# Kernel optimization log

Hardware: AMD Instinct MI355X
Metric: run time of the kernel (lower is better)

The kernel has to match this reference:

```python
import jax, jax.numpy as jnp
import numpy as np


def setup_inputs() -> dict:
    key = jax.random.key(0)
    kq, kk, kv = jax.random.split(key, 3)
    B, L, Q, H, E = 8, 128, 8, 8, 64
    S, P = 128, 8
    queries = jax.random.normal(kq, (B, L, Q, H, E), dtype=jnp.float32)
    keys = jax.random.normal(kk, (B, S, P, H, E), dtype=jnp.float32)
    values = jax.random.normal(kv, (B, S, P, H, E), dtype=jnp.float32)
    attn_mask = jnp.zeros((1,), dtype=bool)  # unused by the module
    return {"queries": queries, "keys": keys, "values": values, "attn_mask": attn_mask}


def reference(queries, keys, values, attn_mask):
    # queries: [B,L,Q,H,E]; keys/values: [B,S,P,H,E]
    B, L, Q, H, E = queries.shape
    S, P = values.shape[1], values.shape[2]
    scale = 1.0 / np.sqrt(E).astype(np.float32)
    # scores: [B,S,P,L,Q,H]
    scores = jnp.einsum('blqhe,bsphe->bsplqh', queries, keys)
    # softmax over joint (S,P) axis
    scaled = (scale * scores).reshape(B, S * P, L, Q, H)
    attn = jax.nn.softmax(scaled, axis=1).reshape(B, S, P, L, Q, H)
    # dropout is identity in eval / with p=0.0
    V = jnp.einsum('bsphe,bsplqh->blqhe', values, attn)
    return V
```

## Files before the change

kernel.cpp:

```cpp
#include <hip/hip_runtime.h>
#include <hip/hip_bf16.h>

typedef __attribute__((ext_vector_type(4))) float f32x4;
typedef __attribute__((ext_vector_type(16))) float f32x16;
typedef __attribute__((ext_vector_type(8))) short bf16x8;
typedef __attribute__((ext_vector_type(4))) unsigned u32x4;

#define MFMA32(a, b, c) __builtin_amdgcn_mfma_f32_32x32x16_bf16(a, b, c, 0, 0, 0)
#define EXP2(x) __builtin_amdgcn_exp2f(x)

constexpr int NQ = 1024;
constexpr int NK = 1024;
constexpr int RS = 512;
constexpr int Ec = 64;
constexpr int KT = 128;
constexpr int NT = NK / KT;
constexpr float QSCALE2 = 0.125f * 1.4426950408889634f;

__device__ __forceinline__ short f2bf(float x) {
    return (short)__builtin_bit_cast(unsigned short, __float2bfloat16(x));
}

__device__ __forceinline__ bf16x8 pack2(float4 a, float4 b) {
    bf16x8 r;
    r[0] = f2bf(a.x); r[1] = f2bf(a.y); r[2] = f2bf(a.z); r[3] = f2bf(a.w);
    r[4] = f2bf(b.x); r[5] = f2bf(b.y); r[6] = f2bf(b.z); r[7] = f2bf(b.w);
    return r;
}

__device__ __forceinline__ bf16x8 pack2s(float4 a, float4 b, float s) {
    bf16x8 r;
    r[0] = f2bf(a.x * s); r[1] = f2bf(a.y * s); r[2] = f2bf(a.z * s); r[3] = f2bf(a.w * s);
    r[4] = f2bf(b.x * s); r[5] = f2bf(b.y * s); r[6] = f2bf(b.z * s); r[7] = f2bf(b.w * s);
    return r;
}

__device__ __forceinline__ unsigned cvtpk(float a, float b) {
    unsigned lo = (unsigned short)__builtin_bit_cast(unsigned short, __float2bfloat16(a));
    unsigned hi = (unsigned short)__builtin_bit_cast(unsigned short, __float2bfloat16(b));
    return lo | (hi << 16);
}

__device__ __forceinline__ void gload16(const short* src, short* dst) {
    __builtin_amdgcn_global_load_lds((const __attribute__((address_space(1))) void*)src,
                                     (__attribute__((address_space(3))) void*)dst, 16, 0, 0);
}

__global__ __launch_bounds__(256, 4)
void cvt_kv(const float* __restrict__ Kg, const float* __restrict__ Vg,
            short* __restrict__ Kbf, short* __restrict__ Vt) {
    __shared__ __attribute__((aligned(16))) short Vl[64][72];
    const int tid  = threadIdx.x;
    const int head = blockIdx.x >> 4;
    const int kb   = blockIdx.x & 15;
    const int b    = head >> 3, h = head & 7;
    const int row  = tid >> 2, q = tid & 3;

    const size_t gin = (((size_t)(b * NK + kb * 64 + row)) * 8 + h) * 64 + q * 16;
    const float4* kp = (const float4*)(Kg + gin);
    float4 k0 = kp[0], k1 = kp[1], k2 = kp[2], k3 = kp[3];
    short* kout = Kbf + ((size_t)head * NK + kb * 64 + row) * 64 + q * 16;
    ((bf16x8*)kout)[0] = pack2(k0, k1);
    ((bf16x8*)kout)[1] = pack2(k2, k3);

    const float4* vp = (const float4*)(Vg + gin);
    float4 v0 = vp[0], v1 = vp[1], v2 = vp[2], v3 = vp[3];
    const float vv[16] = {v0.x, v0.y, v0.z, v0.w, v1.x, v1.y, v1.z, v1.w,
                          v2.x, v2.y, v2.z, v2.w, v3.x, v3.y, v3.z, v3.w};
#pragma unroll
    for (int j = 0; j < 16; ++j) Vl[q * 16 + j][row] = f2bf(vv[j]);
    __syncthreads();
    short* vout = Vt + ((size_t)head * Ec + row) * NK + kb * 64 + q * 16;
    ((bf16x8*)vout)[0] = *(const bf16x8*)&Vl[row][q * 16];
    ((bf16x8*)vout)[1] = *(const bf16x8*)&Vl[row][q * 16 + 8];
}

__global__ __launch_bounds__(512, 2)
void fully_attn_kernel(const float* __restrict__ Qg, const short* __restrict__ Kbf,
                       const short* __restrict__ Vt, float* __restrict__ Og) {
    __shared__ __attribute__((aligned(16))) short Kl[2][KT][64];
    __shared__ __attribute__((aligned(16))) short Vl[2][64][KT];
    __shared__ float scrL[512];

    const int tid  = threadIdx.x;
    const int lane = tid & 63;
    const int wv   = tid >> 6;
    const int grp  = wv & 3;
    const int par  = wv >> 2;
    const int ql   = lane & 31;
    const int hi   = lane >> 5;
    const int swz  = (lane & 7) << 4;

    const int bid  = blockIdx.x;
    const int head = (bid & 7) * 8 + (bid >> 5);
    const int qb   = (bid >> 3) & 3;
    const int b    = head >> 3, h = head & 7;

    const size_t headQ = (size_t)b * NQ * RS + (size_t)h * Ec;
    const short* Kh = Kbf + (size_t)head * NK * Ec;
    const short* Vh = Vt + (size_t)head * Ec * NK;

    const int qrowA = qb * 256 + grp * 64 + ql;
    const int qrowB = qrowA + 32;
    bf16x8 qfA[4], qfB[4];
    {
        const float* qpA = Qg + headQ + (size_t)qrowA * RS;
        const float* qpB = Qg + headQ + (size_t)qrowB * RS;
#pragma unroll
        for (int j = 0; j < 4; ++j) {
            const float4* a4 = (const float4*)(qpA + j * 16 + hi * 8);
            const float4* b4 = (const float4*)(qpB + j * 16 + hi * 8);
            qfA[j] = pack2s(a4[0], a4[1], QSCALE2);
            qfB[j] = pack2s(b4[0], b4[1], QSCALE2);
        }
    }

    const int krow8 = lane >> 3;
    const int kj    = (lane & 7) ^ krow8;
    const int vrow4 = lane >> 4;

#define STAGE_K(buf, tt)                                                          \
    {                                                                             \
        _Pragma("unroll")                                                         \
        for (int s = 0; s < 2; ++s)                                               \
            gload16(Kh + (size_t)((tt) * KT + wv * 16 + s * 8 + krow8) * 64 +     \
                        kj * 8,                                                   \
                    &Kl[buf][wv * 16 + s * 8][0]);                                \
    }

#define STAGE_V(buf, tt)                                                          \
    {                                                                             \
        _Pragma("unroll")                                                         \
        for (int s = 0; s < 2; ++s)                                               \
            gload16(Vh + (size_t)(wv * 8 + s * 4 + vrow4) * NK + (tt) * KT +      \
                        (((lane & 15) ^ ((s * 4 + vrow4) & 7)) * 8),              \
                    &Vl[buf][wv * 8 + s * 4][0]);                                 \
    }

    STAGE_K(0, 0);
    STAGE_V(0, 0);
    __syncthreads();

    float lA = 0.0f, lB = 0.0f;
    f32x16 oA0 = (f32x16)(0.0f), oA1 = (f32x16)(0.0f);
    f32x16 oB0 = (f32x16)(0.0f), oB1 = (f32x16)(0.0f);

    int cur = 0;
    for (int t = 0; t < NT; ++t) {
        if (t + 1 < NT) { STAGE_K(cur ^ 1, t + 1); STAGE_V(cur ^ 1, t + 1); }

        bf16x8 kf[2][4];
#pragma unroll
        for (int kt = 0; kt < 2; ++kt) {
            const char* kr = (const char*)&Kl[cur][par * 64 + kt * 32 + ql][0];
#pragma unroll
            for (int j = 0; j < 4; ++j)
                kf[kt][j] = *(const bf16x8*)(kr + ((j * 32 + hi * 16) ^ swz));
        }
        f32x16 pA[2], pB[2];
        __builtin_amdgcn_s_setprio(1);
#pragma unroll
        for (int kt = 0; kt < 2; ++kt) {
            f32x16 a = (f32x16)(0.0f), bq = (f32x16)(0.0f);
#pragma unroll
            for (int j = 0; j < 4; ++j) {
                a  = MFMA32(kf[kt][j], qfA[j], a);
                bq = MFMA32(kf[kt][j], qfB[j], bq);
            }
            pA[kt] = a;
            pB[kt] = bq;
        }
        __builtin_amdgcn_s_setprio(0);

        bf16x8 vf0[4], vf1[4];
#pragma unroll
        for (int m = 0; m < 4; ++m) {
            const int cb = (par * 128 + m * 32 + hi * 16) ^ swz;
            vf0[m] = *(const bf16x8*)((const char*)&Vl[cur][ql][0] + cb);
            vf1[m] = *(const bf16x8*)((const char*)&Vl[cur][32 + ql][0] + cb);
        }

        {
            float rs0 = 0.f, rs1 = 0.f, rs2 = 0.f, rs3 = 0.f;
#pragma unroll
            for (int kt = 0; kt < 2; ++kt)
#pragma unroll
                for (int i = 0; i < 16; i += 4) {
                    float e0 = EXP2(pA[kt][i + 0]);
                    float e1 = EXP2(pA[kt][i + 1]);
                    float e2 = EXP2(pA[kt][i + 2]);
                    float e3 = EXP2(pA[kt][i + 3]);
                    pA[kt][i + 0] = e0; pA[kt][i + 1] = e1;
                    pA[kt][i + 2] = e2; pA[kt][i + 3] = e3;
                    rs0 += e0; rs1 += e1; rs2 += e2; rs3 += e3;
                }
            lA += (rs0 + rs1) + (rs2 + rs3);
            __builtin_amdgcn_s_setprio(1);
#pragma unroll
            for (int m = 0; m < 4; ++m) {
                const int kt = m >> 1, r0 = (m & 1) * 8;
                unsigned a0 = cvtpk(pA[kt][r0 + 0], pA[kt][r0 + 1]);
                unsigned a1 = cvtpk(pA[kt][r0 + 2], pA[kt][r0 + 3]);
                unsigned b0 = cvtpk(pA[kt][r0 + 4], pA[kt][r0 + 5]);
                unsigned b1 = cvtpk(pA[kt][r0 + 6], pA[kt][r0 + 7]);
                asm("v_permlane32_swap_b32 %0, %1" : "+v"(a0), "+v"(b0));
                asm("v_permlane32_swap_b32 %0, %1" : "+v"(a1), "+v"(b1));
                u32x4 w = {a0, a1, b0, b1};
                bf16x8 pf = __builtin_bit_cast(bf16x8, w);
                oA0 = MFMA32(vf0[m], pf, oA0);
                oA1 = MFMA32(vf1[m], pf, oA1);
            }
            __builtin_amdgcn_s_setprio(0);
        }

        {
            float rs0 = 0.f, rs1 = 0.f, rs2 = 0.f, rs3 = 0.f;
#pragma unroll
            for (int kt = 0; kt < 2; ++kt)
#pragma unroll
                for (int i = 0; i < 16; i += 4) {
                    float e0 = EXP2(pB[kt][i + 0]);
                    float e1 = EXP2(pB[kt][i + 1]);
                    float e2 = EXP2(pB[kt][i + 2]);
                    float e3 = EXP2(pB[kt][i + 3]);
                    pB[kt][i + 0] = e0; pB[kt][i + 1] = e1;
                    pB[kt][i + 2] = e2; pB[kt][i + 3] = e3;
                    rs0 += e0; rs1 += e1; rs2 += e2; rs3 += e3;
                }
            lB += (rs0 + rs1) + (rs2 + rs3);
            __builtin_amdgcn_s_setprio(1);
#pragma unroll
            for (int m = 0; m < 4; ++m) {
                const int kt = m >> 1, r0 = (m & 1) * 8;
                unsigned a0 = cvtpk(pB[kt][r0 + 0], pB[kt][r0 + 1]);
                unsigned a1 = cvtpk(pB[kt][r0 + 2], pB[kt][r0 + 3]);
                unsigned b0 = cvtpk(pB[kt][r0 + 4], pB[kt][r0 + 5]);
                unsigned b1 = cvtpk(pB[kt][r0 + 6], pB[kt][r0 + 7]);
                asm("v_permlane32_swap_b32 %0, %1" : "+v"(a0), "+v"(b0));
                asm("v_permlane32_swap_b32 %0, %1" : "+v"(a1), "+v"(b1));
                u32x4 w = {a0, a1, b0, b1};
                bf16x8 pf = __builtin_bit_cast(bf16x8, w);
                oB0 = MFMA32(vf0[m], pf, oB0);
                oB1 = MFMA32(vf1[m], pf, oB1);
            }
            __builtin_amdgcn_s_setprio(0);
        }

        __syncthreads();
        cur ^= 1;
    }

    lA += __shfl_xor(lA, 32);
    lB += __shfl_xor(lB, 32);

    float* scr = (float*)&Kl[0][0][0];
    const int qslotA = grp * 64 + ql;
    const int qslotB = qslotA + 32;
    if (par == 1) {
#pragma unroll
        for (int i = 0; i < 16; ++i) {
            scr[(hi * 16 + i) * 256 + qslotA]      = oA0[i];
            scr[(32 + hi * 16 + i) * 256 + qslotA] = oA1[i];
            scr[(hi * 16 + i) * 256 + qslotB]      = oB0[i];
            scr[(32 + hi * 16 + i) * 256 + qslotB] = oB1[i];
        }
        if (hi == 0) { scrL[qslotA] = lA; scrL[qslotB] = lB; }
    }
    __syncthreads();
    if (par == 0) {
        const float invA = 1.0f / (lA + scrL[qslotA]);
        const float invB = 1.0f / (lB + scrL[qslotB]);
        float* opA = Og + headQ + (size_t)qrowA * RS;
        float* opB = Og + headQ + (size_t)qrowB * RS;
#pragma unroll
        for (int bnk = 0; bnk < 4; ++bnk) {
            float4 sA0, sA1, sB0, sB1;
#pragma unroll
            for (int j = 0; j < 4; ++j) {
                const int i = bnk * 4 + j;
                ((float*)&sA0)[j] = (oA0[i] + scr[(hi * 16 + i) * 256 + qslotA]) * invA;
                ((float*)&sA1)[j] = (oA1[i] + scr[(32 + hi * 16 + i) * 256 + qslotA]) * invA;
                ((float*)&sB0)[j] = (oB0[i] + scr[(hi * 16 + i) * 256 + qslotB]) * invB;
                ((float*)&sB1)[j] = (oB1[i] + scr[(32 + hi * 16 + i) * 256 + qslotB]) * invB;
            }
            *(float4*)(opA + bnk * 8 + hi * 4)      = sA0;
            *(float4*)(opA + 32 + bnk * 8 + hi * 4) = sA1;
            *(float4*)(opB + bnk * 8 + hi * 4)      = sB0;
            *(float4*)(opB + 32 + bnk * 8 + hi * 4) = sB1;
        }
    }
}

extern "C" void kernel_launch(void* const* d_in, const int* in_sizes, int n_in,
                              void* d_out, int out_size, void* d_ws, size_t ws_size,
                              hipStream_t stream) {
    const float* Qg = (const float*)d_in[0];
    const float* Kg = (const float*)d_in[1];
    const float* Vg = (const float*)d_in[2];
    float* Og = (float*)d_out;

    short* Kbf = (short*)d_ws;
    short* Vt  = (short*)d_ws + (size_t)64 * NK * Ec;

    hipLaunchKernelGGL(cvt_kv, dim3(64 * 16), dim3(256), 0, stream, Kg, Vg, Kbf, Vt);
    hipLaunchKernelGGL(fully_attn_kernel, dim3(256), dim3(512), 0, stream,
                       Qg, Kbf, Vt, Og);
}
```

Before: 45.31 us.

## Halve attention block to 256 threads and double grid to 512 blocks

Each block now handles 128 query rows with 4 waves instead of 256 rows with 8 waves, and the grid doubles to 512 blocks. The K/V staging loops are widened so 4 waves fill the same shared-memory tiles, and the epilogue scratch indexing is resized. The aim is better CU coverage: 256 blocks is about one per CU on this chip, and 512 smaller blocks may balance better. The cost is that each K/V tile is loaded from global memory twice as many times overall, and each wave issues more staging loads.

```diff
diff --git a/kernel.cpp b/kernel.cpp
--- a/kernel.cpp
+++ b/kernel.cpp
@@ -75,32 +75,32 @@
     ((bf16x8*)vout)[1] = *(const bf16x8*)&Vl[row][q * 16 + 8];
 }
 
-__global__ __launch_bounds__(512, 2)
+__global__ __launch_bounds__(256, 2)
 void fully_attn_kernel(const float* __restrict__ Qg, const short* __restrict__ Kbf,
                        const short* __restrict__ Vt, float* __restrict__ Og) {
     __shared__ __attribute__((aligned(16))) short Kl[2][KT][64];
     __shared__ __attribute__((aligned(16))) short Vl[2][64][KT];
-    __shared__ float scrL[512];
+    __shared__ float scrL[128];
 
     const int tid  = threadIdx.x;
     const int lane = tid & 63;
     const int wv   = tid >> 6;
-    const int grp  = wv & 3;
-    const int par  = wv >> 2;
+    const int grp  = wv & 1;
+    const int par  = wv >> 1;
     const int ql   = lane & 31;
     const int hi   = lane >> 5;
     const int swz  = (lane & 7) << 4;
 
     const int bid  = blockIdx.x;
-    const int head = (bid & 7) * 8 + (bid >> 5);
-    const int qb   = (bid >> 3) & 3;
+    const int head = (bid & 7) * 8 + (bid >> 6);
+    const int qb   = (bid >> 3) & 7;
     const int b    = head >> 3, h = head & 7;
 
     const size_t headQ = (size_t)b * NQ * RS + (size_t)h * Ec;
     const short* Kh = Kbf + (size_t)head * NK * Ec;
     const short* Vh = Vt + (size_t)head * Ec * NK;
 
-    const int qrowA = qb * 256 + grp * 64 + ql;
+    const int qrowA = qb * 128 + grp * 64 + ql;
     const int qrowB = qrowA + 32;
     bf16x8 qfA[4], qfB[4];
     {
@@ -115,26 +115,26 @@
         }
     }
 
-    const int krow8 = lane >> 3;
-    const int kj    = (lane & 7) ^ krow8;
-    const int vrow4 = lane >> 4;
+    const int klocal = lane >> 3;
+    const int kj     = (lane & 7) ^ (klocal & 7);
+    const int vlocal = lane >> 4;
 
 #define STAGE_K(buf, tt)                                                          \
     {                                                                             \
         _Pragma("unroll")                                                         \
-        for (int s = 0; s < 2; ++s)                                               \
-            gload16(Kh + (size_t)((tt) * KT + wv * 16 + s * 8 + krow8) * 64 +     \
+        for (int s = 0; s < 4; ++s)                                               \
+            gload16(Kh + (size_t)((tt) * KT + wv * 32 + s * 8 + klocal) * 64 +    \
                         kj * 8,                                                   \
-                    &Kl[buf][wv * 16 + s * 8][0]);                                \
+                    &Kl[buf][wv * 32 + s * 8][0]);                                \
     }
 
 #define STAGE_V(buf, tt)                                                          \
     {                                                                             \
         _Pragma("unroll")                                                         \
-        for (int s = 0; s < 2; ++s)                                               \
-            gload16(Vh + (size_t)(wv * 8 + s * 4 + vrow4) * NK + (tt) * KT +      \
-                        (((lane & 15) ^ ((s * 4 + vrow4) & 7)) * 8),              \
-                    &Vl[buf][wv * 8 + s * 4][0]);                                 \
+        for (int s = 0; s < 4; ++s)                                               \
+            gload16(Vh + (size_t)(wv * 16 + s * 4 + vlocal) * NK + (tt) * KT +    \
+                        (((lane & 15) ^ ((s * 4 + vlocal) & 7)) * 8),             \
+                    &Vl[buf][wv * 16 + s * 4][0]);                                \
     }
 
     STAGE_K(0, 0);
@@ -254,22 +254,22 @@
     lB += __shfl_xor(lB, 32);
 
     float* scr = (float*)&Kl[0][0][0];
-    const int qslotA = grp * 64 + ql;
-    const int qslotB = qslotA + 32;
+    const int slotA = grp * 64 + ql;
+    const int slotB = slotA + 32;
     if (par == 1) {
 #pragma unroll
         for (int i = 0; i < 16; ++i) {
-            scr[(hi * 16 + i) * 256 + qslotA]      = oA0[i];
-            scr[(32 + hi * 16 + i) * 256 + qslotA] = oA1[i];
-            scr[(hi * 16 + i) * 256 + qslotB]      = oB0[i];
-            scr[(32 + hi * 16 + i) * 256 + qslotB] = oB1[i];
-        }
-        if (hi == 0) { scrL[qslotA] = lA; scrL[qslotB] = lB; }
+            scr[(hi * 16 + i) * 128 + slotA]      = oA0[i];
+            scr[(32 + hi * 16 + i) * 128 + slotA] = oA1[i];
+            scr[(hi * 16 + i) * 128 + slotB]      = oB0[i];
+            scr[(32 + hi * 16 + i) * 128 + slotB] = oB1[i];
+        }
+        if (hi == 0) { scrL[slotA] = lA; scrL[slotB] = lB; }
     }
     __syncthreads();
     if (par == 0) {
-        const float invA = 1.0f / (lA + scrL[qslotA]);
-        const float invB = 1.0f / (lB + scrL[qslotB]);
+        const float invA = 1.0f / (lA + scrL[slotA]);
+        const float invB = 1.0f / (lB + scrL[slotB]);
         float* opA = Og + headQ + (size_t)qrowA * RS;
         float* opB = Og + headQ + (size_t)qrowB * RS;
 #pragma unroll
@@ -278,10 +278,10 @@
 #pragma unroll
             for (int j = 0; j < 4; ++j) {
                 const int i = bnk * 4 + j;
-                ((float*)&sA0)[j] = (oA0[i] + scr[(hi * 16 + i) * 256 + qslotA]) * invA;
-                ((float*)&sA1)[j] = (oA1[i] + scr[(32 + hi * 16 + i) * 256 + qslotA]) * invA;
-                ((float*)&sB0)[j] = (oB0[i] + scr[(hi * 16 + i) * 256 + qslotB]) * invB;
-                ((float*)&sB1)[j] = (oB1[i] + scr[(32 + hi * 16 + i) * 256 + qslotB]) * invB;
+                ((float*)&sA0)[j] = (oA0[i] + scr[(hi * 16 + i) * 128 + slotA]) * invA;
+                ((float*)&sA1)[j] = (oA1[i] + scr[(32 + hi * 16 + i) * 128 + slotA]) * invA;
+                ((float*)&sB0)[j] = (oB0[i] + scr[(hi * 16 + i) * 128 + slotB]) * invB;
+                ((float*)&sB1)[j] = (oB1[i] + scr[(32 + hi * 16 + i) * 128 + slotB]) * invB;
             }
             *(float4*)(opA + bnk * 8 + hi * 4)      = sA0;
             *(float4*)(opA + 32 + bnk * 8 + hi * 4) = sA1;
@@ -303,6 +303,6 @@
     short* Vt  = (short*)d_ws + (size_t)64 * NK * Ec;
 
     hipLaunchKernelGGL(cvt_kv, dim3(64 * 16), dim3(256), 0, stream, Kg, Vg, Kbf, Vt);
-    hipLaunchKernelGGL(fully_attn_kernel, dim3(256), dim3(512), 0, stream,
+    hipLaunchKernelGGL(fully_attn_kernel, dim3(512), dim3(256), 0, stream,
                        Qg, Kbf, Vt, Og);
 }
```

After: 45.13 us. Within noise of the previous version (-0.4%).
